# Performance work log

Measured on AMD Instinct MI355X. Metric: run time of the kernel, lower is better.

## Reference

```python
import jax, jax.numpy as jnp
import numpy as np

D_MODEL = 256
NHEAD = 8
DHEAD = D_MODEL // NHEAD
LN_EPS = 1e-5
ATTN_EPS = 1e-6


def layer_norm(x, gamma, beta):
    mu = jnp.mean(x, axis=-1, keepdims=True)
    var = jnp.mean(jnp.square(x - mu), axis=-1, keepdims=True)
    return (x - mu) * jax.lax.rsqrt(var + LN_EPS) * gamma + beta


def setup_inputs() -> dict:
    key = jax.random.key(0)
    ks = jax.random.split(key, 12)
    B, L, S = 8, 4096, 4096
    s = 1.0 / np.sqrt(D_MODEL)
    return {
        "x": jax.random.normal(ks[0], (B, L, D_MODEL), jnp.float32),
        "source": jax.random.normal(ks[1], (B, S, D_MODEL), jnp.float32),
        "wq": jax.random.normal(ks[2], (D_MODEL, D_MODEL), jnp.float32) * s,
        "wk": jax.random.normal(ks[3], (D_MODEL, D_MODEL), jnp.float32) * s,
        "wv": jax.random.normal(ks[4], (D_MODEL, D_MODEL), jnp.float32) * s,
        "wmerge": jax.random.normal(ks[5], (D_MODEL, D_MODEL), jnp.float32) * s,
        "w1": jax.random.normal(ks[6], (2 * D_MODEL, D_MODEL), jnp.float32) * s,
        "w2": jax.random.normal(ks[7], (D_MODEL, 2 * D_MODEL), jnp.float32) * (1.0 / np.sqrt(2 * D_MODEL)),
        "g1": jnp.ones((D_MODEL,), jnp.float32),
        "b1": jnp.zeros((D_MODEL,), jnp.float32),
        "g2": jnp.ones((D_MODEL,), jnp.float32),
        "b2": jnp.zeros((D_MODEL,), jnp.float32),
    }


def reference(x, source, wq, wk, wv, wmerge, w1, w2, g1, b1, g2, b2):
    B, L, _ = x.shape
    S = source.shape[1]
    # QKV projections (bias-free Linear: y = x @ W^T), split into heads
    q = (x @ wq.T).reshape(B, L, NHEAD, DHEAD)
    k = (source @ wk.T).reshape(B, S, NHEAD, DHEAD)
    v = (source @ wv.T).reshape(B, S, NHEAD, DHEAD)
    # LinearAttention (LoFTR): feature map elu(.)+1, kernelized attention
    Q = jax.nn.elu(q) + 1.0
    K = jax.nn.elu(k) + 1.0
    v_len = jnp.asarray(S, v.dtype)
    values = v / v_len
    KV = jnp.einsum('bshd,bshv->bhdv', K, values)        # [B,H,D,D]
    Z = 1.0 / (jnp.einsum('blhd,bhd->blh', Q, K.sum(axis=1)) + ATTN_EPS)
    attended = jnp.einsum('blhd,bhdv,blh->blhv', Q, KV, Z) * v_len
    # merge + residual LN
    message = attended.reshape(B, L, D_MODEL) @ wmerge.T
    x = x + layer_norm(message, g1, b1)
    # MLP (d -> 2d -> d, ReLU) + residual LN
    h = jax.nn.relu(x @ w1.T) @ w2.T
    x = x + layer_norm(h, g2, b2)
    return x
```

## Files before the change

kernel.cpp:

```cpp
#include <hip/hip_runtime.h>

#define DM 256
#define SEQ 4096

typedef __attribute__((ext_vector_type(8))) short bf16x8;
typedef __attribute__((ext_vector_type(4))) float f32x4;

#define MFMA16(a, b, c) __builtin_amdgcn_mfma_f32_16x16x32_bf16(a, b, c, 0, 0, 0)

__device__ __forceinline__ short f2bf(float f) {
    union { float f; unsigned u; } c; c.f = f;
    unsigned r = (c.u + 0x7FFFu + ((c.u >> 16) & 1u)) >> 16;
    return (short)r;
}
__device__ __forceinline__ float bf2f(short s) {
    union { unsigned u; float f; } c; c.u = ((unsigned)(unsigned short)s) << 16; return c.f;
}
__device__ __forceinline__ bf16x8 pack8(float4 a, float4 b) {
    bf16x8 r;
    r[0] = f2bf(a.x); r[1] = f2bf(a.y); r[2] = f2bf(a.z); r[3] = f2bf(a.w);
    r[4] = f2bf(b.x); r[5] = f2bf(b.y); r[6] = f2bf(b.z); r[7] = f2bf(b.w);
    return r;
}

__global__ __launch_bounds__(256) void kWconv(const float* __restrict__ wq, const float* __restrict__ wk,
                                              const float* __restrict__ wv, const float* __restrict__ wm,
                                              const float* __restrict__ w1, const float* __restrict__ w2,
                                              short* __restrict__ dstws) {
    int blk = blockIdx.x;
    const float* src; short* dst;
    if (blk < 32)       { src = wq; dst = dstws;          }
    else if (blk < 64)  { src = wk; dst = dstws + 65536;  blk -= 32; }
    else if (blk < 96)  { src = wv; dst = dstws + 131072; blk -= 64; }
    else if (blk < 128) { src = wm; dst = dstws + 196608; blk -= 96; }
    else if (blk < 192) { src = w1; dst = dstws + 262144; blk -= 128; }
    else                { src = w2; dst = dstws + 393216; blk -= 192; }
    int idx = (blk * 256 + threadIdx.x) * 8;
    float4 f0 = *(const float4*)(src + idx), f1 = *(const float4*)(src + idx + 4);
    *(bf16x8*)(dst + idx) = pack8(f0, f1);
}

__global__ __launch_bounds__(512, 4) void kA(const float* __restrict__ src,
                                             const short* __restrict__ wk, const short* __restrict__ wv,
                                             short* __restrict__ kv_part, float* __restrict__ ksum_part) {
    __shared__ char lds[32768];
    int t = threadIdx.x, lane = t & 63, w = t >> 6, r16 = lane & 15, g = lane >> 4;
    int b = blockIdx.x >> 7, blk = blockIdx.x & 127;
    const float* S = src + ((size_t)b * SEQ + blk * 32) * DM;
#pragma unroll
    for (int i = 0; i < 2; i++) {
        int chunk = t + i * 512, row = chunk >> 5, c8 = chunk & 31;
        const float* p = S + row * DM + c8 * 8;
        float4 f0 = *(const float4*)p, f1 = *(const float4*)(p + 4);
        int by = (row * 512 + c8 * 16) ^ ((row & 7) << 4);
        *(bf16x8*)(lds + by) = pack8(f0, f1);
    }
    __syncthreads();
    f32x4 zz = {0.f, 0.f, 0.f, 0.f};
    f32x4 ak[2][2], av[2][2];
#pragma unroll
    for (int mi = 0; mi < 2; mi++)
#pragma unroll
        for (int ni = 0; ni < 2; ni++) { ak[mi][ni] = zz; av[mi][ni] = zz; }
#pragma unroll
    for (int kt = 0; kt < 8; kt++) {
        bf16x8 A[2];
#pragma unroll
        for (int mi = 0; mi < 2; mi++) {
            int row = mi * 16 + r16;
            A[mi] = *(const bf16x8*)(lds + ((row * 512 + (kt * 32 + g * 8) * 2) ^ ((row & 7) << 4)));
        }
#pragma unroll
        for (int ni = 0; ni < 2; ni++) {
            int n = w * 32 + ni * 16 + r16;
            bf16x8 Bk = *(const bf16x8*)(wk + n * DM + kt * 32 + g * 8);
            bf16x8 Bv = *(const bf16x8*)(wv + n * DM + kt * 32 + g * 8);
#pragma unroll
            for (int mi = 0; mi < 2; mi++) {
                ak[mi][ni] = MFMA16(A[mi], Bk, ak[mi][ni]);
                av[mi][ni] = MFMA16(A[mi], Bv, av[mi][ni]);
            }
        }
    }
    __syncthreads();
    char* kT = lds + w * 4096;
    char* vT = kT + 2048;
    float ksp[2] = {0.f, 0.f};
#pragma unroll
    for (int mi = 0; mi < 2; mi++)
#pragma unroll
        for (int ni = 0; ni < 2; ni++)
#pragma unroll
            for (int j = 0; j < 4; j++) {
                float q = ak[mi][ni][j];
                float e = q > 0.f ? q + 1.f : __expf(q);
                ksp[ni] += e;
                int srow = mi * 16 + g * 4 + j, feat = ni * 16 + r16;
                int by = feat * 64 + srow * 2;
                *(short*)(kT + by) = f2bf(e);
                *(short*)(vT + by) = f2bf(av[mi][ni][j]);
            }
    __syncthreads();
    f32x4 kv[2][2];
#pragma unroll
    for (int vi = 0; vi < 2; vi++)
#pragma unroll
        for (int di = 0; di < 2; di++) kv[vi][di] = zz;
    {
        bf16x8 Af[2], Bf[2];
#pragma unroll
        for (int vi = 0; vi < 2; vi++) {
            int row = vi * 16 + r16;
            Af[vi] = *(const bf16x8*)(vT + row * 64 + g * 16);
            Bf[vi] = *(const bf16x8*)(kT + row * 64 + g * 16);
        }
#pragma unroll
        for (int vi = 0; vi < 2; vi++)
#pragma unroll
            for (int di = 0; di < 2; di++) kv[vi][di] = MFMA16(Af[vi], Bf[di], kv[vi][di]);
    }
    short* kvp = kv_part + ((size_t)(b * 128 + blk) * 8 + w) * 1024;
#pragma unroll
    for (int vi = 0; vi < 2; vi++)
#pragma unroll
        for (int di = 0; di < 2; di++)
#pragma unroll
            for (int j = 0; j < 4; j++) {
                int v = vi * 16 + g * 4 + j, d = di * 16 + r16;
                kvp[v * 32 + d] = f2bf(kv[vi][di][j]);
            }
#pragma unroll
    for (int ni = 0; ni < 2; ni++) {
        ksp[ni] += __shfl_xor(ksp[ni], 16);
        ksp[ni] += __shfl_xor(ksp[ni], 32);
    }
    if (lane < 16) {
        float* kp = ksum_part + (size_t)(b * 128 + blk) * 256 + w * 32;
#pragma unroll
        for (int ni = 0; ni < 2; ni++) kp[ni * 16 + lane] = ksp[ni];
    }
}

__global__ __launch_bounds__(256) void kA2(const short* __restrict__ kv_part, const float* __restrict__ ksum_part,
                                           short* __restrict__ kvt_bf, float* __restrict__ ksum4) {
    int blk = blockIdx.x, t = threadIdx.x;
    int b = blk >> 5, h = (blk >> 2) & 7, q = blk & 3;
    int e = q * 256 + t;
    float s0 = 0.f, s1 = 0.f, s2 = 0.f, s3 = 0.f;
    for (int bk = 0; bk < 128; bk += 4) {
        s0 += bf2f(kv_part[((size_t)(b * 128 + bk) * 8 + h) * 1024 + e]);
        s1 += bf2f(kv_part[((size_t)(b * 128 + bk + 1) * 8 + h) * 1024 + e]);
        s2 += bf2f(kv_part[((size_t)(b * 128 + bk + 2) * 8 + h) * 1024 + e]);
        s3 += bf2f(kv_part[((size_t)(b * 128 + bk + 3) * 8 + h) * 1024 + e]);
    }
    kvt_bf[(size_t)(b * 8 + h) * 1024 + e] = f2bf((s0 + s1) + (s2 + s3));
    if (t < 32) {
        float s = 0.f;
        for (int bk = q * 32; bk < q * 32 + 32; bk++)
            s += ksum_part[(size_t)(b * 128 + bk) * 256 + h * 32 + t];
        ksum4[((b * 8 + h) * 4 + q) * 32 + t] = s;
    }
}

__global__ __launch_bounds__(512, 4) void kBC(const float* __restrict__ x,
                                              const short* __restrict__ wq_bf, const short* __restrict__ wm_bf,
                                              const short* __restrict__ w1_bf, const short* __restrict__ w2_bf,
                                              const short* __restrict__ kvt_bf, const float* __restrict__ ksum4,
                                              const float* __restrict__ g1, const float* __restrict__ b1,
                                              const float* __restrict__ g2, const float* __restrict__ b2,
                                              float* __restrict__ out) {
    __shared__ char lds[35840];
    char* xt = lds;
    char* qa = lds + 16384;
    float* red = (float*)(lds + 32768);
    float* ksl = (float*)(lds + 34816);
    int t = threadIdx.x, lane = t & 63, w = t >> 6, r16 = lane & 15, g = lane >> 4;
    int b = blockIdx.x >> 7, lb = blockIdx.x & 127, l0 = lb * 32;
    const float* xb = x + ((size_t)b * SEQ + l0) * DM;
#pragma unroll
    for (int i = 0; i < 2; i++) {
        int chunk = t + i * 512, row = chunk >> 5, c8 = chunk & 31;
        const float* p = xb + row * DM + c8 * 8;
        float4 f0 = *(const float4*)p, f1 = *(const float4*)(p + 4);
        int by = (row * 512 + c8 * 16) ^ ((row & 7) << 4);
        *(bf16x8*)(xt + by) = pack8(f0, f1);
    }
    if (t < 256) {
        int h = t >> 5, d = t & 31;
        const float* kp = ksum4 + (size_t)((b * 8 + h) * 4) * 32 + d;
        ksl[t] = (kp[0] + kp[32]) + (kp[64] + kp[96]);
    }
    __syncthreads();
    f32x4 zz = {0.f, 0.f, 0.f, 0.f};
    f32x4 acc[2][2];
#pragma unroll
    for (int mi = 0; mi < 2; mi++)
#pragma unroll
        for (int ni = 0; ni < 2; ni++) acc[mi][ni] = zz;
#pragma unroll
    for (int kt = 0; kt < 8; kt++) {
        bf16x8 A[2], Bf[2];
#pragma unroll
        for (int mi = 0; mi < 2; mi++) {
            int row = mi * 16 + r16;
            A[mi] = *(const bf16x8*)(xt + ((row * 512 + (kt * 32 + g * 8) * 2) ^ ((row & 7) << 4)));
        }
#pragma unroll
        for (int ni = 0; ni < 2; ni++)
            Bf[ni] = *(const bf16x8*)(wq_bf + (w * 32 + ni * 16 + r16) * DM + kt * 32 + g * 8);
#pragma unroll
        for (int mi = 0; mi < 2; mi++)
#pragma unroll
            for (int ni = 0; ni < 2; ni++) acc[mi][ni] = MFMA16(A[mi], Bf[ni], acc[mi][ni]);
    }
    float ks0 = ksl[w * 32 + r16], ks1 = ksl[w * 32 + 16 + r16];
    float Zr[2][4];
#pragma unroll
    for (int mi = 0; mi < 2; mi++)
#pragma unroll
        for (int j = 0; j < 4; j++) {
#pragma unroll
            for (int ni = 0; ni < 2; ni++) {
                float q = acc[mi][ni][j];
                acc[mi][ni][j] = q > 0.f ? q + 1.f : __expf(q);
            }
            float d0 = acc[mi][0][j] * ks0 + acc[mi][1][j] * ks1;
#pragma unroll
            for (int m = 1; m < 16; m <<= 1) d0 += __shfl_xor(d0, m);
            Zr[mi][j] = 1.f / (d0 + 1e-6f);
        }
#pragma unroll
    for (int mi = 0; mi < 2; mi++)
#pragma unroll
        for (int ni = 0; ni < 2; ni++)
#pragma unroll
            for (int j = 0; j < 4; j++) {
                int row = mi * 16 + g * 4 + j, col = w * 32 + ni * 16 + r16;
                *(short*)(qa + ((row * 512 + col * 2) ^ ((row & 7) << 4))) = f2bf(acc[mi][ni][j]);
            }
    f32x4 at[2][2];
#pragma unroll
    for (int mi = 0; mi < 2; mi++)
#pragma unroll
        for (int vi = 0; vi < 2; vi++) at[mi][vi] = zz;
    {
        bf16x8 A2[2], B2[2];
#pragma unroll
        for (int mi = 0; mi < 2; mi++) {
            int row = mi * 16 + r16, col = w * 32 + g * 8;
            A2[mi] = *(const bf16x8*)(qa + ((row * 512 + col * 2) ^ ((row & 7) << 4)));
        }
        const short* kvb = kvt_bf + (size_t)(b * 8 + w) * 1024;
#pragma unroll
        for (int vi = 0; vi < 2; vi++)
            B2[vi] = *(const bf16x8*)(kvb + (vi * 16 + r16) * 32 + g * 8);
#pragma unroll
        for (int mi = 0; mi < 2; mi++)
#pragma unroll
            for (int vi = 0; vi < 2; vi++) at[mi][vi] = MFMA16(A2[mi], B2[vi], at[mi][vi]);
    }
#pragma unroll
    for (int mi = 0; mi < 2; mi++)
#pragma unroll
        for (int vi = 0; vi < 2; vi++)
#pragma unroll
            for (int j = 0; j < 4; j++) {
                int row = mi * 16 + g * 4 + j, col = w * 32 + vi * 16 + r16;
                *(short*)(qa + ((row * 512 + col * 2) ^ ((row & 7) << 4))) = f2bf(at[mi][vi][j] * Zr[mi][j]);
            }
    __syncthreads();
    f32x4 am[2][2];
#pragma unroll
    for (int mi = 0; mi < 2; mi++)
#pragma unroll
        for (int ni = 0; ni < 2; ni++) am[mi][ni] = zz;
#pragma unroll
    for (int kt = 0; kt < 8; kt++) {
        bf16x8 A[2], Bf[2];
#pragma unroll
        for (int mi = 0; mi < 2; mi++) {
            int row = mi * 16 + r16;
            A[mi] = *(const bf16x8*)(qa + ((row * 512 + (kt * 32 + g * 8) * 2) ^ ((row & 7) << 4)));
        }
#pragma unroll
        for (int ni = 0; ni < 2; ni++)
            Bf[ni] = *(const bf16x8*)(wm_bf + (w * 32 + ni * 16 + r16) * DM + kt * 32 + g * 8);
#pragma unroll
        for (int mi = 0; mi < 2; mi++)
#pragma unroll
            for (int ni = 0; ni < 2; ni++) am[mi][ni] = MFMA16(A[mi], Bf[ni], am[mi][ni]);
    }
#pragma unroll
    for (int mi = 0; mi < 2; mi++)
#pragma unroll
        for (int j = 0; j < 4; j++) {
            float s = am[mi][0][j] + am[mi][1][j];
            float s2 = am[mi][0][j] * am[mi][0][j] + am[mi][1][j] * am[mi][1][j];
#pragma unroll
            for (int m = 1; m < 16; m <<= 1) { s += __shfl_xor(s, m); s2 += __shfl_xor(s2, m); }
            if (r16 == 0) { int row = mi * 16 + g * 4 + j; red[(row * 8 + w) * 2] = s; red[(row * 8 + w) * 2 + 1] = s2; }
        }
    __syncthreads();
    {
        float g1v[2], b1v[2];
#pragma unroll
        for (int ni = 0; ni < 2; ni++) { int col = w * 32 + ni * 16 + r16; g1v[ni] = g1[col]; b1v[ni] = b1[col]; }
#pragma unroll
        for (int mi = 0; mi < 2; mi++)
#pragma unroll
            for (int j = 0; j < 4; j++) {
                int row = mi * 16 + g * 4 + j;
                float mu = 0.f, ex2 = 0.f;
#pragma unroll
                for (int ww = 0; ww < 8; ww++) { mu += red[(row * 8 + ww) * 2]; ex2 += red[(row * 8 + ww) * 2 + 1]; }
                mu *= (1.f / DM); ex2 *= (1.f / DM);
                float rstd = rsqrtf(ex2 - mu * mu + 1e-5f);
#pragma unroll
                for (int ni = 0; ni < 2; ni++) {
                    int col = w * 32 + ni * 16 + r16;
                    int by = (row * 512 + col * 2) ^ ((row & 7) << 4);
                    float xv = bf2f(*(const short*)(xt + by));
                    *(short*)(xt + by) = f2bf(xv + (am[mi][ni][j] - mu) * rstd * g1v[ni] + b1v[ni]);
                }
            }
    }
    __syncthreads();
    f32x4 a2[2][2];
#pragma unroll
    for (int mi = 0; mi < 2; mi++)
#pragma unroll
        for (int ni = 0; ni < 2; ni++) a2[mi][ni] = zz;
#pragma unroll
    for (int hf = 0; hf < 2; hf++) {
        f32x4 a1[2][2];
#pragma unroll
        for (int mi = 0; mi < 2; mi++)
#pragma unroll
            for (int ni = 0; ni < 2; ni++) a1[mi][ni] = zz;
#pragma unroll
        for (int kt = 0; kt < 8; kt++) {
            bf16x8 A[2], Bf[2];
#pragma unroll
            for (int mi = 0; mi < 2; mi++) {
                int row = mi * 16 + r16;
                A[mi] = *(const bf16x8*)(xt + ((row * 512 + (kt * 32 + g * 8) * 2) ^ ((row & 7) << 4)));
            }
#pragma unroll
            for (int ni = 0; ni < 2; ni++)
                Bf[ni] = *(const bf16x8*)(w1_bf + (hf * 256 + w * 32 + ni * 16 + r16) * DM + kt * 32 + g * 8);
#pragma unroll
            for (int mi = 0; mi < 2; mi++)
#pragma unroll
                for (int ni = 0; ni < 2; ni++) a1[mi][ni] = MFMA16(A[mi], Bf[ni], a1[mi][ni]);
        }
#pragma unroll
        for (int mi = 0; mi < 2; mi++)
#pragma unroll
            for (int ni = 0; ni < 2; ni++)
#pragma unroll
                for (int j = 0; j < 4; j++) {
                    float hv = a1[mi][ni][j]; hv = hv > 0.f ? hv : 0.f;
                    int row = mi * 16 + g * 4 + j, col = w * 32 + ni * 16 + r16;
                    *(short*)(qa + ((row * 512 + col * 2) ^ ((row & 7) << 4))) = f2bf(hv);
                }
        __syncthreads();
#pragma unroll
        for (int kt = 0; kt < 8; kt++) {
            bf16x8 A[2], Bf[2];
#pragma unroll
            for (int mi = 0; mi < 2; mi++) {
                int row = mi * 16 + r16;
                A[mi] = *(const bf16x8*)(qa + ((row * 512 + (kt * 32 + g * 8) * 2) ^ ((row & 7) << 4)));
            }
#pragma unroll
            for (int ni = 0; ni < 2; ni++)
                Bf[ni] = *(const bf16x8*)(w2_bf + (w * 32 + ni * 16 + r16) * 512 + hf * 256 + kt * 32 + g * 8);
#pragma unroll
            for (int mi = 0; mi < 2; mi++)
#pragma unroll
                for (int ni = 0; ni < 2; ni++) a2[mi][ni] = MFMA16(A[mi], Bf[ni], a2[mi][ni]);
        }
        __syncthreads();
    }
#pragma unroll
    for (int mi = 0; mi < 2; mi++)
#pragma unroll
        for (int j = 0; j < 4; j++) {
            float s = a2[mi][0][j] + a2[mi][1][j];
            float s2 = a2[mi][0][j] * a2[mi][0][j] + a2[mi][1][j] * a2[mi][1][j];
#pragma unroll
            for (int m = 1; m < 16; m <<= 1) { s += __shfl_xor(s, m); s2 += __shfl_xor(s2, m); }
            if (r16 == 0) { int row = mi * 16 + g * 4 + j; red[(row * 8 + w) * 2] = s; red[(row * 8 + w) * 2 + 1] = s2; }
        }
    __syncthreads();
    {
        float g2v[2], b2v[2];
#pragma unroll
        for (int ni = 0; ni < 2; ni++) { int col = w * 32 + ni * 16 + r16; g2v[ni] = g2[col]; b2v[ni] = b2[col]; }
        float* op = out + ((size_t)b * SEQ + l0) * DM;
#pragma unroll
        for (int mi = 0; mi < 2; mi++)
#pragma unroll
            for (int j = 0; j < 4; j++) {
                int row = mi * 16 + g * 4 + j;
                float mu = 0.f, ex2 = 0.f;
#pragma unroll
                for (int ww = 0; ww < 8; ww++) { mu += red[(row * 8 + ww) * 2]; ex2 += red[(row * 8 + ww) * 2 + 1]; }
                mu *= (1.f / DM); ex2 *= (1.f / DM);
                float rstd = rsqrtf(ex2 - mu * mu + 1e-5f);
#pragma unroll
                for (int ni = 0; ni < 2; ni++) {
                    int col = w * 32 + ni * 16 + r16;
                    float xv = bf2f(*(const short*)(xt + ((row * 512 + col * 2) ^ ((row & 7) << 4))));
                    op[row * DM + col] = xv + (a2[mi][ni][j] - mu) * rstd * g2v[ni] + b2v[ni];
                }
            }
    }
}

extern "C" void kernel_launch(void* const* d_in, const int* in_sizes, int n_in,
                              void* d_out, int out_size, void* d_ws, size_t ws_size,
                              hipStream_t stream) {
    const float* x   = (const float*)d_in[0];
    const float* src = (const float*)d_in[1];
    const float* wq  = (const float*)d_in[2];
    const float* wk  = (const float*)d_in[3];
    const float* wv  = (const float*)d_in[4];
    const float* wm  = (const float*)d_in[5];
    const float* w1  = (const float*)d_in[6];
    const float* w2  = (const float*)d_in[7];
    const float* g1  = (const float*)d_in[8];
    const float* b1  = (const float*)d_in[9];
    const float* g2  = (const float*)d_in[10];
    const float* b2  = (const float*)d_in[11];
    float* out = (float*)d_out;

    char* ws = (char*)d_ws;
    short* w_bf      = (short*)ws;
    short* kvt_bf    = (short*)(ws + 1048576);
    float* ksum4     = (float*)(ws + 1179648);
    short* kv_part   = (short*)(ws + 1212416);
    float* ksum_part = (float*)(ws + 17989632);

    kWconv<<<256, 256, 0, stream>>>(wq, wk, wv, wm, w1, w2, w_bf);
    kA<<<1024, 512, 0, stream>>>(src, w_bf + 65536, w_bf + 131072, kv_part, ksum_part);
    kA2<<<256, 256, 0, stream>>>(kv_part, ksum_part, kvt_bf, ksum4);
    kBC<<<1024, 512, 0, stream>>>(x, w_bf, w_bf + 196608, w_bf + 262144, w_bf + 393216,
                                  kvt_bf, ksum4, g1, b1, g2, b2, out);
}
```

Before: 258.4 us.

## Double rows per block to 64 and use padded LDS strides

Each block of kA and kBC now handles 64 sequence rows instead of 32, so every bf16 weight fragment loaded from global memory feeds twice as many MFMAs, and the number of KV partials reduced in kA2 is halved. The XOR swizzle on the LDS tiles is replaced with padded row strides (528 and 144 bytes) to avoid bank conflicts with simpler addressing. The cost is roughly double the LDS per block and more accumulator registers, which lowers occupancy, and only 512 blocks are launched, which may leave the GPU's compute units less evenly loaded.

```diff
diff --git a/kernel.cpp b/kernel.cpp
--- a/kernel.cpp
+++ b/kernel.cpp
@@ -2,6 +2,8 @@
 
 #define DM 256
 #define SEQ 4096
+#define XSTR 528
+#define KSTR 144
 
 typedef __attribute__((ext_vector_type(8))) short bf16x8;
 typedef __attribute__((ext_vector_type(4))) float f32x4;
@@ -43,51 +45,50 @@
 __global__ __launch_bounds__(512, 4) void kA(const float* __restrict__ src,
                                              const short* __restrict__ wk, const short* __restrict__ wv,
                                              short* __restrict__ kv_part, float* __restrict__ ksum_part) {
-    __shared__ char lds[32768];
+    __shared__ char lds[73728];
     int t = threadIdx.x, lane = t & 63, w = t >> 6, r16 = lane & 15, g = lane >> 4;
-    int b = blockIdx.x >> 7, blk = blockIdx.x & 127;
-    const float* S = src + ((size_t)b * SEQ + blk * 32) * DM;
-#pragma unroll
-    for (int i = 0; i < 2; i++) {
+    int b = blockIdx.x >> 6, blk = blockIdx.x & 63;
+    const float* S = src + ((size_t)b * SEQ + blk * 64) * DM;
+#pragma unroll
+    for (int i = 0; i < 4; i++) {
         int chunk = t + i * 512, row = chunk >> 5, c8 = chunk & 31;
         const float* p = S + row * DM + c8 * 8;
         float4 f0 = *(const float4*)p, f1 = *(const float4*)(p + 4);
-        int by = (row * 512 + c8 * 16) ^ ((row & 7) << 4);
-        *(bf16x8*)(lds + by) = pack8(f0, f1);
+        *(bf16x8*)(lds + row * XSTR + c8 * 16) = pack8(f0, f1);
     }
     __syncthreads();
     f32x4 zz = {0.f, 0.f, 0.f, 0.f};
-    f32x4 ak[2][2], av[2][2];
-#pragma unroll
-    for (int mi = 0; mi < 2; mi++)
+    f32x4 ak[4][2], av[4][2];
+#pragma unroll
+    for (int mi = 0; mi < 4; mi++)
 #pragma unroll
         for (int ni = 0; ni < 2; ni++) { ak[mi][ni] = zz; av[mi][ni] = zz; }
+    const char* aB0 = lds + r16 * XSTR + g * 16;
+    const short* wkB0 = wk + (w * 32 + r16) * DM + g * 8;
+    const short* wvB0 = wv + (w * 32 + r16) * DM + g * 8;
 #pragma unroll
     for (int kt = 0; kt < 8; kt++) {
-        bf16x8 A[2];
-#pragma unroll
-        for (int mi = 0; mi < 2; mi++) {
-            int row = mi * 16 + r16;
-            A[mi] = *(const bf16x8*)(lds + ((row * 512 + (kt * 32 + g * 8) * 2) ^ ((row & 7) << 4)));
-        }
+        bf16x8 A[4];
+#pragma unroll
+        for (int mi = 0; mi < 4; mi++)
+            A[mi] = *(const bf16x8*)(aB0 + mi * (16 * XSTR) + kt * 64);
 #pragma unroll
         for (int ni = 0; ni < 2; ni++) {
-            int n = w * 32 + ni * 16 + r16;
-            bf16x8 Bk = *(const bf16x8*)(wk + n * DM + kt * 32 + g * 8);
-            bf16x8 Bv = *(const bf16x8*)(wv + n * DM + kt * 32 + g * 8);
-#pragma unroll
-            for (int mi = 0; mi < 2; mi++) {
+            bf16x8 Bk = *(const bf16x8*)(wkB0 + ni * (16 * DM) + kt * 32);
+            bf16x8 Bv = *(const bf16x8*)(wvB0 + ni * (16 * DM) + kt * 32);
+#pragma unroll
+            for (int mi = 0; mi < 4; mi++) {
                 ak[mi][ni] = MFMA16(A[mi], Bk, ak[mi][ni]);
                 av[mi][ni] = MFMA16(A[mi], Bv, av[mi][ni]);
             }
         }
     }
     __syncthreads();
-    char* kT = lds + w * 4096;
-    char* vT = kT + 2048;
+    char* kT = lds + w * 9216;
+    char* vT = kT + 4608;
     float ksp[2] = {0.f, 0.f};
 #pragma unroll
-    for (int mi = 0; mi < 2; mi++)
+    for (int mi = 0; mi < 4; mi++)
 #pragma unroll
         for (int ni = 0; ni < 2; ni++)
 #pragma unroll
@@ -96,7 +97,7 @@
                 float e = q > 0.f ? q + 1.f : __expf(q);
                 ksp[ni] += e;
                 int srow = mi * 16 + g * 4 + j, feat = ni * 16 + r16;
-                int by = feat * 64 + srow * 2;
+                int by = feat * KSTR + srow * 2;
                 *(short*)(kT + by) = f2bf(e);
                 *(short*)(vT + by) = f2bf(av[mi][ni][j]);
             }
@@ -107,19 +108,23 @@
 #pragma unroll
         for (int di = 0; di < 2; di++) kv[vi][di] = zz;
     {
-        bf16x8 Af[2], Bf[2];
-#pragma unroll
-        for (int vi = 0; vi < 2; vi++) {
-            int row = vi * 16 + r16;
-            Af[vi] = *(const bf16x8*)(vT + row * 64 + g * 16);
-            Bf[vi] = *(const bf16x8*)(kT + row * 64 + g * 16);
-        }
-#pragma unroll
-        for (int vi = 0; vi < 2; vi++)
-#pragma unroll
-            for (int di = 0; di < 2; di++) kv[vi][di] = MFMA16(Af[vi], Bf[di], kv[vi][di]);
-    }
-    short* kvp = kv_part + ((size_t)(b * 128 + blk) * 8 + w) * 1024;
+        const char* vB = vT + r16 * KSTR + g * 16;
+        const char* kB = kT + r16 * KSTR + g * 16;
+#pragma unroll
+        for (int st = 0; st < 2; st++) {
+            bf16x8 Af[2], Bf[2];
+#pragma unroll
+            for (int vi = 0; vi < 2; vi++) {
+                Af[vi] = *(const bf16x8*)(vB + vi * (16 * KSTR) + st * 64);
+                Bf[vi] = *(const bf16x8*)(kB + vi * (16 * KSTR) + st * 64);
+            }
+#pragma unroll
+            for (int vi = 0; vi < 2; vi++)
+#pragma unroll
+                for (int di = 0; di < 2; di++) kv[vi][di] = MFMA16(Af[vi], Bf[di], kv[vi][di]);
+        }
+    }
+    short* kvp = kv_part + ((size_t)(b * 64 + blk) * 8 + w) * 1024;
 #pragma unroll
     for (int vi = 0; vi < 2; vi++)
 #pragma unroll
@@ -135,7 +140,7 @@
         ksp[ni] += __shfl_xor(ksp[ni], 32);
     }
     if (lane < 16) {
-        float* kp = ksum_part + (size_t)(b * 128 + blk) * 256 + w * 32;
+        float* kp = ksum_part + (size_t)(b * 64 + blk) * 256 + w * 32;
 #pragma unroll
         for (int ni = 0; ni < 2; ni++) kp[ni * 16 + lane] = ksp[ni];
     }
@@ -147,17 +152,17 @@
     int b = blk >> 5, h = (blk >> 2) & 7, q = blk & 3;
     int e = q * 256 + t;
     float s0 = 0.f, s1 = 0.f, s2 = 0.f, s3 = 0.f;
-    for (int bk = 0; bk < 128; bk += 4) {
-        s0 += bf2f(kv_part[((size_t)(b * 128 + bk) * 8 + h) * 1024 + e]);
-        s1 += bf2f(kv_part[((size_t)(b * 128 + bk + 1) * 8 + h) * 1024 + e]);
-        s2 += bf2f(kv_part[((size_t)(b * 128 + bk + 2) * 8 + h) * 1024 + e]);
-        s3 += bf2f(kv_part[((size_t)(b * 128 + bk + 3) * 8 + h) * 1024 + e]);
+    for (int bk = 0; bk < 64; bk += 4) {
+        s0 += bf2f(kv_part[((size_t)(b * 64 + bk) * 8 + h) * 1024 + e]);
+        s1 += bf2f(kv_part[((size_t)(b * 64 + bk + 1) * 8 + h) * 1024 + e]);
+        s2 += bf2f(kv_part[((size_t)(b * 64 + bk + 2) * 8 + h) * 1024 + e]);
+        s3 += bf2f(kv_part[((size_t)(b * 64 + bk + 3) * 8 + h) * 1024 + e]);
     }
     kvt_bf[(size_t)(b * 8 + h) * 1024 + e] = f2bf((s0 + s1) + (s2 + s3));
     if (t < 32) {
         float s = 0.f;
-        for (int bk = q * 32; bk < q * 32 + 32; bk++)
-            s += ksum_part[(size_t)(b * 128 + bk) * 256 + h * 32 + t];
+        for (int bk = q * 16; bk < q * 16 + 16; bk++)
+            s += ksum_part[(size_t)(b * 64 + bk) * 256 + h * 32 + t];
         ksum4[((b * 8 + h) * 4 + q) * 32 + t] = s;
     }
 }
@@ -169,21 +174,20 @@
                                               const float* __restrict__ g1, const float* __restrict__ b1,
                                               const float* __restrict__ g2, const float* __restrict__ b2,
                                               float* __restrict__ out) {
-    __shared__ char lds[35840];
+    __shared__ char lds[72704];
     char* xt = lds;
-    char* qa = lds + 16384;
-    float* red = (float*)(lds + 32768);
-    float* ksl = (float*)(lds + 34816);
+    char* qa = lds + 33792;
+    float* red = (float*)(lds + 67584);
+    float* ksl = (float*)(lds + 71680);
     int t = threadIdx.x, lane = t & 63, w = t >> 6, r16 = lane & 15, g = lane >> 4;
-    int b = blockIdx.x >> 7, lb = blockIdx.x & 127, l0 = lb * 32;
+    int b = blockIdx.x >> 6, lb = blockIdx.x & 63, l0 = lb * 64;
     const float* xb = x + ((size_t)b * SEQ + l0) * DM;
 #pragma unroll
-    for (int i = 0; i < 2; i++) {
+    for (int i = 0; i < 4; i++) {
         int chunk = t + i * 512, row = chunk >> 5, c8 = chunk & 31;
         const float* p = xb + row * DM + c8 * 8;
         float4 f0 = *(const float4*)p, f1 = *(const float4*)(p + 4);
-        int by = (row * 512 + c8 * 16) ^ ((row & 7) << 4);
-        *(bf16x8*)(xt + by) = pack8(f0, f1);
+        *(bf16x8*)(xt + row * XSTR + c8 * 16) = pack8(f0, f1);
     }
     if (t < 256) {
         int h = t >> 5, d = t & 31;
@@ -192,31 +196,34 @@
     }
     __syncthreads();
     f32x4 zz = {0.f, 0.f, 0.f, 0.f};
-    f32x4 acc[2][2];
-#pragma unroll
-    for (int mi = 0; mi < 2; mi++)
+    const char* aXB = xt + r16 * XSTR + g * 16;
+    const char* aQB = qa + r16 * XSTR + g * 16;
+    f32x4 acc[4][2];
+#pragma unroll
+    for (int mi = 0; mi < 4; mi++)
 #pragma unroll
         for (int ni = 0; ni < 2; ni++) acc[mi][ni] = zz;
-#pragma unroll
-    for (int kt = 0; kt < 8; kt++) {
-        bf16x8 A[2], Bf[2];
-#pragma unroll
-        for (int mi = 0; mi < 2; mi++) {
-            int row = mi * 16 + r16;
-            A[mi] = *(const bf16x8*)(xt + ((row * 512 + (kt * 32 + g * 8) * 2) ^ ((row & 7) << 4)));
-        }
-#pragma unroll
-        for (int ni = 0; ni < 2; ni++)
-            Bf[ni] = *(const bf16x8*)(wq_bf + (w * 32 + ni * 16 + r16) * DM + kt * 32 + g * 8);
-#pragma unroll
-        for (int mi = 0; mi < 2; mi++)
-#pragma unroll
-            for (int ni = 0; ni < 2; ni++) acc[mi][ni] = MFMA16(A[mi], Bf[ni], acc[mi][ni]);
+    {
+        const short* wqB = wq_bf + (w * 32 + r16) * DM + g * 8;
+#pragma unroll
+        for (int kt = 0; kt < 8; kt++) {
+            bf16x8 A[4], Bf[2];
+#pragma unroll
+            for (int mi = 0; mi < 4; mi++)
+                A[mi] = *(const bf16x8*)(aXB + mi * (16 * XSTR) + kt * 64);
+#pragma unroll
+            for (int ni = 0; ni < 2; ni++)
+                Bf[ni] = *(const bf16x8*)(wqB + ni * (16 * DM) + kt * 32);
+#pragma unroll
+            for (int mi = 0; mi < 4; mi++)
+#pragma unroll
+                for (int ni = 0; ni < 2; ni++) acc[mi][ni] = MFMA16(A[mi], Bf[ni], acc[mi][ni]);
+        }
     }
     float ks0 = ksl[w * 32 + r16], ks1 = ksl[w * 32 + 16 + r16];
-    float Zr[2][4];
-#pragma unroll
-    for (int mi = 0; mi < 2; mi++)
+    float Zr[4][4];
+#pragma unroll
+    for (int mi = 0; mi < 4; mi++)
 #pragma unroll
         for (int j = 0; j < 4; j++) {
 #pragma unroll
@@ -230,68 +237,67 @@
             Zr[mi][j] = 1.f / (d0 + 1e-6f);
         }
 #pragma unroll
-    for (int mi = 0; mi < 2; mi++)
+    for (int mi = 0; mi < 4; mi++)
 #pragma unroll
         for (int ni = 0; ni < 2; ni++)
 #pragma unroll
             for (int j = 0; j < 4; j++) {
                 int row = mi * 16 + g * 4 + j, col = w * 32 + ni * 16 + r16;
-                *(short*)(qa + ((row * 512 + col * 2) ^ ((row & 7) << 4))) = f2bf(acc[mi][ni][j]);
-            }
-    f32x4 at[2][2];
-#pragma unroll
-    for (int mi = 0; mi < 2; mi++)
+                *(short*)(qa + row * XSTR + col * 2) = f2bf(acc[mi][ni][j]);
+            }
+    f32x4 at[4][2];
+#pragma unroll
+    for (int mi = 0; mi < 4; mi++)
 #pragma unroll
         for (int vi = 0; vi < 2; vi++) at[mi][vi] = zz;
     {
-        bf16x8 A2[2], B2[2];
-#pragma unroll
-        for (int mi = 0; mi < 2; mi++) {
-            int row = mi * 16 + r16, col = w * 32 + g * 8;
-            A2[mi] = *(const bf16x8*)(qa + ((row * 512 + col * 2) ^ ((row & 7) << 4)));
-        }
+        bf16x8 A2[4], B2[2];
+#pragma unroll
+        for (int mi = 0; mi < 4; mi++)
+            A2[mi] = *(const bf16x8*)(qa + (mi * 16 + r16) * XSTR + (w * 32 + g * 8) * 2);
         const short* kvb = kvt_bf + (size_t)(b * 8 + w) * 1024;
 #pragma unroll
         for (int vi = 0; vi < 2; vi++)
             B2[vi] = *(const bf16x8*)(kvb + (vi * 16 + r16) * 32 + g * 8);
 #pragma unroll
-        for (int mi = 0; mi < 2; mi++)
+        for (int mi = 0; mi < 4; mi++)
 #pragma unroll
             for (int vi = 0; vi < 2; vi++) at[mi][vi] = MFMA16(A2[mi], B2[vi], at[mi][vi]);
     }
 #pragma unroll
-    for (int mi = 0; mi < 2; mi++)
+    for (int mi = 0; mi < 4; mi++)
 #pragma unroll
         for (int vi = 0; vi < 2; vi++)
 #pragma unroll
             for (int j = 0; j < 4; j++) {
                 int row = mi * 16 + g * 4 + j, col = w * 32 + vi * 16 + r16;
-                *(short*)(qa + ((row * 512 + col * 2) ^ ((row & 7) << 4))) = f2bf(at[mi][vi][j] * Zr[mi][j]);
-            }
-    __syncthreads();
-    f32x4 am[2][2];
-#pragma unroll
-    for (int mi = 0; mi < 2; mi++)
+                *(short*)(qa + row * XSTR + col * 2) = f2bf(at[mi][vi][j] * Zr[mi][j]);
+            }
+    __syncthreads();
+    f32x4 am[4][2];
+#pragma unroll
+    for (int mi = 0; mi < 4; mi++)
 #pragma unroll
         for (int ni = 0; ni < 2; ni++) am[mi][ni] = zz;
-#pragma unroll
-    for (int kt = 0; kt < 8; kt++) {
-        bf16x8 A[2], Bf[2];
-#pragma unroll
-        for (int mi = 0; mi < 2; mi++) {
-            int row = mi * 16 + r16;
-            A[mi] = *(const bf16x8*)(qa + ((row * 512 + (kt * 32 + g * 8) * 2) ^ ((row & 7) << 4)));
-        }
-#pragma unroll
-        for (int ni = 0; ni < 2; ni++)
-            Bf[ni] = *(const bf16x8*)(wm_bf + (w * 32 + ni * 16 + r16) * DM + kt * 32 + g * 8);
-#pragma unroll
-        for (int mi = 0; mi < 2; mi++)
-#pragma unroll
-            for (int ni = 0; ni < 2; ni++) am[mi][ni] = MFMA16(A[mi], Bf[ni], am[mi][ni]);
-    }
-#pragma unroll
-    for (int mi = 0; mi < 2; mi++)
+    {
+        const short* wmB = wm_bf + (w * 32 + r16) * DM + g * 8;
+#pragma unroll
+        for (int kt = 0; kt < 8; kt++) {
+            bf16x8 A[4], Bf[2];
+#pragma unroll
+            for (int mi = 0; mi < 4; mi++)
+                A[mi] = *(const bf16x8*)(aQB + mi * (16 * XSTR) + kt * 64);
+#pragma unroll
+            for (int ni = 0; ni < 2; ni++)
+                Bf[ni] = *(const bf16x8*)(wmB + ni * (16 * DM) + kt * 32);
+#pragma unroll
+            for (int mi = 0; mi < 4; mi++)
+#pragma unroll
+                for (int ni = 0; ni < 2; ni++) am[mi][ni] = MFMA16(A[mi], Bf[ni], am[mi][ni]);
+        }
+    }
+#pragma unroll
+    for (int mi = 0; mi < 4; mi++)
 #pragma unroll
         for (int j = 0; j < 4; j++) {
             float s = am[mi][0][j] + am[mi][1][j];
@@ -306,7 +312,7 @@
 #pragma unroll
         for (int ni = 0; ni < 2; ni++) { int col = w * 32 + ni * 16 + r16; g1v[ni] = g1[col]; b1v[ni] = b1[col]; }
 #pragma unroll
-        for (int mi = 0; mi < 2; mi++)
+        for (int mi = 0; mi < 4; mi++)
 #pragma unroll
             for (int j = 0; j < 4; j++) {
                 int row = mi * 16 + g * 4 + j;
@@ -318,72 +324,74 @@
 #pragma unroll
                 for (int ni = 0; ni < 2; ni++) {
                     int col = w * 32 + ni * 16 + r16;
-                    int by = (row * 512 + col * 2) ^ ((row & 7) << 4);
-                    float xv = bf2f(*(const short*)(xt + by));
-                    *(short*)(xt + by) = f2bf(xv + (am[mi][ni][j] - mu) * rstd * g1v[ni] + b1v[ni]);
+                    char* bp = xt + row * XSTR + col * 2;
+                    float xv = bf2f(*(const short*)bp);
+                    *(short*)bp = f2bf(xv + (am[mi][ni][j] - mu) * rstd * g1v[ni] + b1v[ni]);
                 }
             }
     }
     __syncthreads();
-    f32x4 a2[2][2];
-#pragma unroll
-    for (int mi = 0; mi < 2; mi++)
+    f32x4 a2[4][2];
+#pragma unroll
+    for (int mi = 0; mi < 4; mi++)
 #pragma unroll
         for (int ni = 0; ni < 2; ni++) a2[mi][ni] = zz;
 #pragma unroll
     for (int hf = 0; hf < 2; hf++) {
-        f32x4 a1[2][2];
-#pragma unroll
-        for (int mi = 0; mi < 2; mi++)
+        f32x4 a1[4][2];
+#pragma unroll
+        for (int mi = 0; mi < 4; mi++)
 #pragma unroll
             for (int ni = 0; ni < 2; ni++) a1[mi][ni] = zz;
-#pragma unroll
-        for (int kt = 0; kt < 8; kt++) {
-            bf16x8 A[2], Bf[2];
-#pragma unroll
-            for (int mi = 0; mi < 2; mi++) {
-                int row = mi * 16 + r16;
-                A[mi] = *(const bf16x8*)(xt + ((row * 512 + (kt * 32 + g * 8) * 2) ^ ((row & 7) << 4)));
-            }
-#pragma unroll
-            for (int ni = 0; ni < 2; ni++)
-                Bf[ni] = *(const bf16x8*)(w1_bf + (hf * 256 + w * 32 + ni * 16 + r16) * DM + kt * 32 + g * 8);
-#pragma unroll
-            for (int mi = 0; mi < 2; mi++)
-#pragma unroll
-                for (int ni = 0; ni < 2; ni++) a1[mi][ni] = MFMA16(A[mi], Bf[ni], a1[mi][ni]);
-        }
-#pragma unroll
-        for (int mi = 0; mi < 2; mi++)
+        {
+            const short* w1B = w1_bf + (hf * 256 + w * 32 + r16) * DM + g * 8;
+#pragma unroll
+            for (int kt = 0; kt < 8; kt++) {
+                bf16x8 A[4], Bf[2];
+#pragma unroll
+                for (int mi = 0; mi < 4; mi++)
+                    A[mi] = *(const bf16x8*)(aXB + mi * (16 * XSTR) + kt * 64);
+#pragma unroll
+                for (int ni = 0; ni < 2; ni++)
+                    Bf[ni] = *(const bf16x8*)(w1B + ni * (16 * DM) + kt * 32);
+#pragma unroll
+                for (int mi = 0; mi < 4; mi++)
+#pragma unroll
+                    for (int ni = 0; ni < 2; ni++) a1[mi][ni] = MFMA16(A[mi], Bf[ni], a1[mi][ni]);
+            }
+        }
+#pragma unroll
+        for (int mi = 0; mi < 4; mi++)
 #pragma unroll
             for (int ni = 0; ni < 2; ni++)
 #pragma unroll
                 for (int j = 0; j < 4; j++) {
                     float hv = a1[mi][ni][j]; hv = hv > 0.f ? hv : 0.f;
                     int row = mi * 16 + g * 4 + j, col = w * 32 + ni * 16 + r16;
-                    *(short*)(qa + ((row * 512 + col * 2) ^ ((row & 7) << 4))) = f2bf(hv);
+                    *(short*)(qa + row * XSTR + col * 2) = f2bf(hv);
                 }
         __syncthreads();
-#pragma unroll
-        for (int kt = 0; kt < 8; kt++) {
-            bf16x8 A[2], Bf[2];
-#pragma unroll
-            for (int mi = 0; mi < 2; mi++) {
-                int row = mi * 16 + r16;
-                A[mi] = *(const bf16x8*)(qa + ((row * 512 + (kt * 32 + g * 8) * 2) ^ ((row & 7) << 4)));
-            }
-#pragma unroll
-            for (int ni = 0; ni < 2; ni++)
-                Bf[ni] = *(const bf16x8*)(w2_bf + (w * 32 + ni * 16 + r16) * 512 + hf * 256 + kt * 32 + g * 8);
-#pragma unroll
-            for (int mi = 0; mi < 2; mi++)
-#pragma unroll
-                for (int ni = 0; ni < 2; ni++) a2[mi][ni] = MFMA16(A[mi], Bf[ni], a2[mi][ni]);
+        {
+            const short* w2B = w2_bf + (w * 32 + r16) * 512 + hf * 256 + g * 8;
+#pragma unroll
+            for (int kt = 0; kt < 8; kt++) {
+                bf16x8 A[4], Bf[2];
+#pragma unroll
+                for (int mi = 0; mi < 4; mi++)
+                    A[mi] = *(const bf16x8*)(aQB + mi * (16 * XSTR) + kt * 64);
+#pragma unroll
+                for (int ni = 0; ni < 2; ni++)
+                    Bf[ni] = *(const bf16x8*)(w2B + ni * (16 * 512) + kt * 32);
+#pragma unroll
+                for (int mi = 0; mi < 4; mi++)
+#pragma unroll
+                    for (int ni = 0; ni < 2; ni++) a2[mi][ni] = MFMA16(A[mi], Bf[ni], a2[mi][ni]);
+            }
         }
         __syncthreads();
     }
 #pragma unroll
-    for (int mi = 0; mi < 2; mi++)
+    for (int mi = 0; mi < 4; mi++)
 #pragma unroll
         for (int j = 0; j < 4; j++) {
             float s = a2[mi][0][j] + a2[mi][1][j];
@@ -399,7 +407,7 @@
         for (int ni = 0; ni < 2; ni++) { int col = w * 32 + ni * 16 + r16; g2v[ni] = g2[col]; b2v[ni] = b2[col]; }
         float* op = out + ((size_t)b * SEQ + l0) * DM;
 #pragma unroll
-        for (int mi = 0; mi < 2; mi++)
+        for (int mi = 0; mi < 4; mi++)
 #pragma unroll
             for (int j = 0; j < 4; j++) {
                 int row = mi * 16 + g * 4 + j;
@@ -411,7 +419,7 @@
 #pragma unroll
                 for (int ni = 0; ni < 2; ni++) {
                     int col = w * 32 + ni * 16 + r16;
-                    float xv = bf2f(*(const short*)(xt + ((row * 512 + col * 2) ^ ((row & 7) << 4))));
+                    float xv = bf2f(*(const short*)(xt + row * XSTR + col * 2));
                     op[row * DM + col] = xv + (a2[mi][ni][j] - mu) * rstd * g2v[ni] + b2v[ni];
                 }
             }
@@ -440,11 +448,11 @@
     short* kvt_bf    = (short*)(ws + 1048576);
     float* ksum4     = (float*)(ws + 1179648);
     short* kv_part   = (short*)(ws + 1212416);
-    float* ksum_part = (float*)(ws + 17989632);
+    float* ksum_part = (float*)(ws + 9601024);
 
     kWconv<<<256, 256, 0, stream>>>(wq, wk, wv, wm, w1, w2, w_bf);
-    kA<<<1024, 512, 0, stream>>>(src, w_bf + 65536, w_bf + 131072, kv_part, ksum_part);
+    kA<<<512, 512, 0, stream>>>(src, w_bf + 65536, w_bf + 131072, kv_part, ksum_part);
     kA2<<<256, 256, 0, stream>>>(kv_part, ksum_part, kvt_bf, ksum4);
-    kBC<<<1024, 512, 0, stream>>>(x, w_bf, w_bf + 196608, w_bf + 262144, w_bf + 393216,
-                                  kvt_bf, ksum4, g1, b1, g2, b2, out);
-}
+    kBC<<<512, 512, 0, stream>>>(x, w_bf, w_bf + 196608, w_bf + 262144, w_bf + 393216,
+                                 kvt_bf, ksum4, g1, b1, g2, b2, out);
+}
```

Result: faster. 215.6 us (-16.6%).
